# Kernel optimization log

Hardware: AMD Instinct MI355X
Metric: run time of the kernel (lower is better)

The kernel has to match this reference:

```python
import jax, jax.numpy as jnp
import numpy as np

BS, T, X_DIM = 16, 4096, 256


def setup_inputs() -> dict:
    key = jax.random.key(0)
    kx, kb, kl = jax.random.split(key, 3)
    x_set = jax.random.normal(kx, (BS, T, X_DIM), dtype=jnp.float32)
    # Match torch.nn.init.orthogonal_ via QR of a Gaussian matrix
    B, _ = jnp.linalg.qr(jax.random.normal(kb, (X_DIM, X_DIM), dtype=jnp.float32))
    Lam, _ = jnp.linalg.qr(jax.random.normal(kl, (X_DIM, X_DIM), dtype=jnp.float32))
    return {"x_set": x_set, "B": B.astype(jnp.float32), "Lam": Lam.astype(jnp.float32)}


def reference(x_set, B, Lam):
    # Original computes h_T = sum_{j=0}^{T} Lambda^j @ B @ x_{T-j} (O(T^2)).
    # Equivalent linear recurrence: h_t = Lambda @ h_{t-1} + B @ x_t, h_{-1} = 0.
    Bx = jnp.einsum('de,bte->btd', B, x_set)          # [bs, T, d]

    def step(h, bx_t):
        h = jnp.einsum('de,be->bd', Lam, h) + bx_t    # [bs, d]
        return h, h

    h0 = jnp.zeros((x_set.shape[0], x_set.shape[2]), dtype=x_set.dtype)
    _, hs = jax.lax.scan(step, h0, jnp.swapaxes(Bx, 0, 1))  # [T, bs, d]
    return jnp.swapaxes(hs, 0, 1)                            # [bs, T, d]
```

## Files before the change

### kernel.cpp

```cpp
#include <hip/hip_runtime.h>
#include <hip/hip_bf16.h>
#include <stdint.h>


#define CHUNK  64
#define NCHUNK 64

typedef short v8s __attribute__((ext_vector_type(8)));
typedef float v4f __attribute__((ext_vector_type(4)));

static __device__ __forceinline__ unsigned short f2u(float f) {
  union { float f; unsigned int u; } x; x.f = f;
  unsigned int u = x.u + 0x7FFFu + ((x.u >> 16) & 1u);
  return (unsigned short)(u >> 16);
}
static __device__ __forceinline__ float u2f(unsigned short h) {
  union { unsigned int u; float f; } x; x.u = ((unsigned int)h) << 16;
  return x.f;
}
static __device__ __forceinline__ void lds_barrier() {
  asm volatile("s_waitcnt lgkmcnt(0)\n\ts_barrier" ::: "memory");
}

template<bool A_F32, bool C_BF16, bool ADD_C>
__global__ __launch_bounds__(256) void gemm_tile(
    const void* __restrict__ Ap, const unsigned short* __restrict__ Bp,
    void* __restrict__ Cp, int lda, int ldb, int ldc, int Kper, long csplit)
{
  __shared__ unsigned short As[64][72];
  __shared__ unsigned short Bst[64][72];
  const int tid = threadIdx.x;
  const int lane = tid & 63, w = tid >> 6;
  const int q = lane >> 4, ln = lane & 15;
  const long n0 = (long)blockIdx.x * 64;
  const long m0 = (long)blockIdx.y * 64;
  const int  kz = blockIdx.z;
  const long kbase = (long)kz * Kper;
  const int sm = tid >> 2;
  const int sk = (tid & 3) << 4;

  v4f acc[4];
#pragma unroll
  for (int i = 0; i < 4; ++i) acc[i] = 0;

  float4 fA[4];
  v8s aR0, aR1, bR0, bR1;

  auto load_tile = [&](long kg) {
    if (A_F32) {
      const float* A = (const float*)Ap + (m0 + sm) * (long)lda + kg + sk;
#pragma unroll
      for (int t = 0; t < 4; ++t) fA[t] = ((const float4*)A)[t];
    } else {
      const unsigned short* A = (const unsigned short*)Ap + (m0 + sm) * (long)lda + kg + sk;
      aR0 = ((const v8s*)A)[0]; aR1 = ((const v8s*)A)[1];
    }
    const unsigned short* Bg = Bp + (kg + sm) * (long)ldb + n0 + sk;
    bR0 = ((const v8s*)Bg)[0]; bR1 = ((const v8s*)Bg)[1];
  };

  load_tile(kbase);

  for (int ks = 0; ks < Kper; ks += 64) {
    __syncthreads();
    if (A_F32) {
      unsigned short* d = &As[sm][sk];
#pragma unroll
      for (int t = 0; t < 4; ++t) {
        d[4*t+0] = f2u(fA[t].x); d[4*t+1] = f2u(fA[t].y);
        d[4*t+2] = f2u(fA[t].z); d[4*t+3] = f2u(fA[t].w);
      }
    } else {
      *(v8s*)&As[sm][sk] = aR0; *(v8s*)&As[sm][sk + 8] = aR1;
    }
#pragma unroll
    for (int r = 0; r < 8; ++r) Bst[sk + r][sm] = (unsigned short)bR0[r];
#pragma unroll
    for (int r = 0; r < 8; ++r) Bst[sk + 8 + r][sm] = (unsigned short)bR1[r];
    __syncthreads();
    if (ks + 64 < Kper) load_tile(kbase + ks + 64);
#pragma unroll
    for (int kb = 0; kb < 64; kb += 32) {
      v8s a = *(const v8s*)&As[w*16 + ln][kb + q*8];
#pragma unroll
      for (int nb = 0; nb < 4; ++nb) {
        v8s b = *(const v8s*)&Bst[nb*16 + ln][kb + q*8];
        acc[nb] = __builtin_amdgcn_mfma_f32_16x16x32_bf16(a, b, acc[nb], 0, 0, 0);
      }
    }
  }
#pragma unroll
  for (int nb = 0; nb < 4; ++nb)
#pragma unroll
    for (int r = 0; r < 4; ++r) {
      const long row = m0 + w*16 + q*4 + r;
      const long col = n0 + nb*16 + ln;
      float v = acc[nb][r];
      if (C_BF16) ((unsigned short*)Cp)[row * (long)ldc + col] = f2u(v);
      else {
        float* Cf = (float*)Cp + (long)kz * csplit;
        if (ADD_C) v += Cf[row * (long)ldc + col];
        Cf[row * (long)ldc + col] = v;
      }
    }
}

__global__ __launch_bounds__(256) void pow_round(
    unsigned short* __restrict__ Phi, unsigned short* __restrict__ Plo, int mpow)
{
  __shared__ unsigned short As[64][72];
  __shared__ unsigned short Bst[64][72];
  const int tid = threadIdx.x, lane = tid & 63, w = tid >> 6;
  const int q = lane >> 4, ln = lane & 15;
  const int jj = (blockIdx.x >> 2) + 1;
  const int n0 = (blockIdx.x & 3) * 64;
  const int m0 = blockIdx.y * 64;
  const unsigned short* Ah = Phi + (size_t)mpow * 65536;
  const unsigned short* Al = Plo + (size_t)mpow * 65536;
  const unsigned short* Bh = Phi + (size_t)jj * 65536;
  const unsigned short* Bl = Plo + (size_t)jj * 65536;
  const int sm = tid >> 2, sk = (tid & 3) << 4;
  v4f acc[4];
#pragma unroll
  for (int i = 0; i < 4; ++i) acc[i] = 0;

  v8s aR0, aR1, bR0, bR1;
  auto load_tile = [&](int it) {
    const int seg = it >> 2, ks = (it & 3) << 6;
    const unsigned short* Asrc = (seg == 1) ? Al : Ah;
    const unsigned short* Bsrc = (seg == 2) ? Bl : Bh;
    const unsigned short* Ag = Asrc + (size_t)(m0 + sm) * 256 + ks + sk;
    aR0 = ((const v8s*)Ag)[0]; aR1 = ((const v8s*)Ag)[1];
    const unsigned short* Bg = Bsrc + (size_t)(ks + sm) * 256 + n0 + sk;
    bR0 = ((const v8s*)Bg)[0]; bR1 = ((const v8s*)Bg)[1];
  };

  load_tile(0);
  for (int it = 0; it < 12; ++it) {
    __syncthreads();
    *(v8s*)&As[sm][sk] = aR0; *(v8s*)&As[sm][sk + 8] = aR1;
#pragma unroll
    for (int r = 0; r < 8; ++r) Bst[sk + r][sm] = (unsigned short)bR0[r];
#pragma unroll
    for (int r = 0; r < 8; ++r) Bst[sk + 8 + r][sm] = (unsigned short)bR1[r];
    __syncthreads();
    if (it + 1 < 12) load_tile(it + 1);
#pragma unroll
    for (int kb = 0; kb < 64; kb += 32) {
      v8s a = *(const v8s*)&As[w*16 + ln][kb + q*8];
#pragma unroll
      for (int nb = 0; nb < 4; ++nb) {
        v8s bb = *(const v8s*)&Bst[nb*16 + ln][kb + q*8];
        acc[nb] = __builtin_amdgcn_mfma_f32_16x16x32_bf16(a, bb, acc[nb], 0, 0, 0);
      }
    }
  }
  const size_t ob = (size_t)(mpow + jj) * 65536;
#pragma unroll
  for (int nb = 0; nb < 4; ++nb)
#pragma unroll
    for (int r = 0; r < 4; ++r) {
      const int row = m0 + w*16 + q*4 + r;
      const int col = n0 + nb*16 + ln;
      float v = acc[nb][r];
      unsigned short hi = f2u(v);
      Phi[ob + (size_t)row*256 + col] = hi;
      Plo[ob + (size_t)row*256 + col] = f2u(v - u2f(hi));
    }
}

__global__ __launch_bounds__(256) void pack_init(
    const float* __restrict__ Bm, const float* __restrict__ Lam,
    unsigned short* __restrict__ Bt, unsigned short* __restrict__ LamT,
    unsigned short* __restrict__ Phi, unsigned short* __restrict__ Plo)
{
  const int idx = blockIdx.x * 256 + threadIdx.x;
  const int e = idx >> 8, d = idx & 255;
  Bt[idx]   = f2u(Bm[d * 256 + e]);
  LamT[idx] = f2u(Lam[d * 256 + e]);
  float v = Lam[idx];
  unsigned short hi = f2u(v);
  Phi[65536 + idx] = hi;
  Plo[65536 + idx] = f2u(v - u2f(hi));
  const int dd = idx >> 8, ee = idx & 255;
  Phi[idx] = (dd == ee) ? (unsigned short)0x3F80 : (unsigned short)0;
  Plo[idx] = 0;
}

__global__ __launch_bounds__(256) void pack2_init(
    const unsigned short* __restrict__ Phi, const unsigned short* __restrict__ Plo,
    unsigned short* __restrict__ Phi2, unsigned short* __restrict__ Plo2)
{
  const int idx = blockIdx.x * 256 + threadIdx.x;
  const int dd = idx >> 8, ee = idx & 255;
  Phi2[idx] = (dd == ee) ? (unsigned short)0x3F80 : (unsigned short)0;
  Plo2[idx] = 0;
  Phi2[65536 + idx] = Phi[(size_t)64 * 65536 + idx];
  Plo2[65536 + idx] = Plo[(size_t)64 * 65536 + idx];
}

__global__ __launch_bounds__(256) void pack_all(
    const unsigned short* __restrict__ Phi,
    const unsigned short* __restrict__ Phi2, const unsigned short* __restrict__ Plo2,
    unsigned short* __restrict__ Ghat, unsigned short* __restrict__ Q,
    unsigned short* __restrict__ Qcat, unsigned short* __restrict__ G2,
    unsigned short* __restrict__ LcT2hi, unsigned short* __restrict__ LcT2lo)
{
  __shared__ unsigned short tile[64][65];
  const int tx = threadIdx.x & 63, ty = threadIdx.x >> 6;
  const int blk0 = blockIdx.x;
  if (blk0 < 2048) {
    const int blk = blk0;
    int t16, jpar;
    const unsigned short* src;
    if (blk < 1024) { jpar = blk >> 4;            t16 = blk & 15;  src = Phi + (size_t)(63 - jpar) * 65536; }
    else            { int v = blk - 1024; jpar = v >> 4; t16 = v & 15; src = Phi + (size_t)(jpar + 1) * 65536; }
    const int d0 = (t16 & 3) * 64, e0 = (t16 >> 2) * 64;
#pragma unroll
    for (int s = 0; s < 16; ++s)
      tile[ty*16 + s][tx] = src[(size_t)(d0 + ty*16 + s) * 256 + e0 + tx];
    __syncthreads();
    if (blk < 1024) {
#pragma unroll
      for (int s = 0; s < 16; ++s) {
        const int e = e0 + ty*16 + s, d = d0 + tx;
        Ghat[((size_t)(jpar*256 + e)) * 256 + d] = tile[tx][ty*16 + s];
      }
    } else {
#pragma unroll
      for (int s = 0; s < 16; ++s) {
        const int e = e0 + ty*16 + s, d = d0 + tx;
        Q[(size_t)e * 16384 + jpar*256 + d] = tile[tx][ty*16 + s];
      }
    }
    return;
  }
  const int blk = blk0 - 2048;
  if (blk < 1152) {
    const int rt = blk >> 5, ct = blk & 31;
    const int k0 = rt * 64, c0 = ct * 64;
    const int r = c0 >> 8, d0 = c0 & 255;
    int p = 0, e0 = 0;
    bool zero = false;
    if (k0 < 256) { p = r; e0 = k0; }
    else {
      const int u = (k0 - 256) >> 8; e0 = (k0 - 256) & 255;
      if (u >= r) zero = true; else p = r - 1 - u;
    }
    if (zero) {
#pragma unroll
      for (int s = 0; s < 16; ++s)
        Qcat[(size_t)(k0 + ty*16 + s) * 2048 + c0 + tx] = 0;
      return;
    }
    const unsigned short* src = Phi2 + (size_t)p * 65536;
#pragma unroll
    for (int s = 0; s < 16; ++s)
      tile[ty*16 + s][tx] = src[(size_t)(d0 + ty*16 + s) * 256 + e0 + tx];
    __syncthreads();
#pragma unroll
    for (int s = 0; s < 16; ++s)
      Qcat[(size_t)(k0 + ty*16 + s) * 2048 + c0 + tx] = tile[tx][ty*16 + s];
  } else if (blk < 1280) {
    const int t = blk - 1152;
    const int rt = t >> 2, ct = t & 3;
    const int k0 = rt * 64, d0 = ct * 64;
    const int r = k0 >> 8, e0 = k0 & 255;
    const unsigned short* src = Phi2 + (size_t)(7 - r) * 65536;
#pragma unroll
    for (int s = 0; s < 16; ++s)
      tile[ty*16 + s][tx] = src[(size_t)(d0 + ty*16 + s) * 256 + e0 + tx];
    __syncthreads();
#pragma unroll
    for (int s = 0; s < 16; ++s)
      G2[(size_t)(k0 + ty*16 + s) * 256 + d0 + tx] = tile[tx][ty*16 + s];
  } else {
    const int t = blk - 1280;
    const int half = t >> 4, t16 = t & 15;
    const int d0 = (t16 & 3) * 64, e0 = (t16 >> 2) * 64;
    const unsigned short* src = (half ? Plo2 : Phi2) + (size_t)8 * 65536;
    unsigned short* dst = half ? LcT2lo : LcT2hi;
#pragma unroll
    for (int s = 0; s < 16; ++s)
      tile[ty*16 + s][tx] = src[(size_t)(d0 + ty*16 + s) * 256 + e0 + tx];
    __syncthreads();
#pragma unroll
    for (int s = 0; s < 16; ++s)
      dst[(size_t)(e0 + ty*16 + s) * 256 + d0 + tx] = tile[tx][ty*16 + s];
  }
}

__global__ __launch_bounds__(256) void reduce_s2(
    const float* __restrict__ Sp, unsigned short* __restrict__ Acat)
{
  const int f = blockIdx.x * 256 + threadIdx.x;
  float v = 0;
#pragma unroll
  for (int z = 0; z < 8; ++z) v += Sp[(size_t)z * 262144 + f];
  const int e = f & 255, i = (f >> 8) & 63, b = f >> 14;
  const int u = i & 7, m = i >> 3;
  Acat[(size_t)(b*8 + m) * 2304 + 256 + u*256 + e] = f2u(v);
}

__global__ __launch_bounds__(512, 2) void k4b_combine(
    const unsigned short* __restrict__ LcT2hi, const unsigned short* __restrict__ LcT2lo,
    const float* __restrict__ S2, unsigned short* __restrict__ Acat)
{
  __shared__ unsigned short Hhi[16][264];
  __shared__ unsigned short Hlo[16][264];
  const int tid = threadIdx.x, lane = tid & 63, w = tid >> 6;
  const int q = lane >> 4, ln = lane & 15;

  v8s bhi[8][2], blo[8][2];
#pragma unroll
  for (int kk = 0; kk < 8; ++kk)
#pragma unroll
    for (int nb = 0; nb < 2; ++nb) {
      const int n = 32*w + nb*16 + ln;
#pragma unroll
      for (int r = 0; r < 8; ++r) {
        const int k = kk*32 + q*8 + r;
        bhi[kk][nb][r] = (short)LcT2hi[k*256 + n];
        blo[kk][nb][r] = (short)LcT2lo[k*256 + n];
      }
    }
  for (int e = tid; e < 16*264; e += 512) { (&Hhi[0][0])[e] = 0; (&Hlo[0][0])[e] = 0; }
  lds_barrier();

  for (int m = 0; m < 8; ++m) {
    for (int e = tid; e < 4096; e += 512) {
      const int b = e >> 8, d = e & 255;
      Acat[(size_t)(b*8 + m) * 2304 + d] = Hhi[b][d];
    }
    v8s ahi[8], alo[8];
#pragma unroll
    for (int kk = 0; kk < 8; ++kk) {
      ahi[kk] = *(const v8s*)&Hhi[ln][kk*32 + q*8];
      alo[kk] = *(const v8s*)&Hlo[ln][kk*32 + q*8];
    }
    lds_barrier();
    v4f acc[2];
#pragma unroll
    for (int nb = 0; nb < 2; ++nb)
#pragma unroll
      for (int r = 0; r < 4; ++r) {
        const int bb = 4*q + r, col = 32*w + nb*16 + ln;
        acc[nb][r] = S2[(size_t)(bb*8 + m) * 256 + col];
      }
#pragma unroll
    for (int kk = 0; kk < 8; ++kk)
#pragma unroll
      for (int nb = 0; nb < 2; ++nb) {
        acc[nb] = __builtin_amdgcn_mfma_f32_16x16x32_bf16(ahi[kk], bhi[kk][nb], acc[nb], 0, 0, 0);
        acc[nb] = __builtin_amdgcn_mfma_f32_16x16x32_bf16(alo[kk], bhi[kk][nb], acc[nb], 0, 0, 0);
        acc[nb] = __builtin_amdgcn_mfma_f32_16x16x32_bf16(ahi[kk], blo[kk][nb], acc[nb], 0, 0, 0);
      }
#pragma unroll
    for (int nb = 0; nb < 2; ++nb)
#pragma unroll
      for (int r = 0; r < 4; ++r) {
        const int bb = 4*q + r, col = 32*w + nb*16 + ln;
        float v = acc[nb][r];
        unsigned short hi = f2u(v);
        Hhi[bb][col] = hi;
        Hlo[bb][col] = f2u(v - u2f(hi));
      }
    lds_barrier();
  }
}

__global__ __launch_bounds__(256, 1) void k5_scan(
    const unsigned short* __restrict__ LamT,
    const unsigned short* __restrict__ Bx, float* __restrict__ Out)
{
  __shared__ unsigned short gs[2][16][264];
  const int tid = threadIdx.x, lane = tid & 63, w = tid >> 6;
  const int q = lane >> 4, ln = lane & 15;
  const int blk = blockIdx.x;
  const int b  = blk >> 4;
  const int i0 = (blk * 4) & 63;

  v8s bf[8][4];
#pragma unroll
  for (int kk = 0; kk < 8; ++kk)
#pragma unroll
    for (int nb = 0; nb < 4; ++nb) {
      const int n = 64*w + nb*16 + ln;
#pragma unroll
      for (int r = 0; r < 8; ++r)
        bf[kk][nb][r] = (short)LamT[(kk*32 + q*8 + r) * 256 + n];
    }
  for (int e = tid; e < 16*264; e += 256) (&gs[0][0][0])[e] = 0;

  size_t base[4];
#pragma unroll
  for (int r = 0; r < 4; ++r)
    base[r] = ((size_t)b*4096 + (size_t)(i0 + r)*64) * 256;
  const int colw = 64*w;

  unsigned short bxr[2][4][4];
  if (q == 0) {
#pragma unroll
    for (int s = 0; s < 2; ++s)
#pragma unroll
      for (int r = 0; r < 4; ++r)
#pragma unroll
        for (int nb = 0; nb < 4; ++nb)
          bxr[s][r][nb] = Bx[base[r] + (size_t)s*256 + colw + nb*16 + ln];
  }
  lds_barrier();

#pragma unroll 2
  for (int j = 0; j < CHUNK; ++j) {
    v8s a[8];
#pragma unroll
    for (int kk = 0; kk < 8; ++kk) a[kk] = *(const v8s*)&gs[j & 1][ln][kk*32 + q*8];
    v4f acc[4];
#pragma unroll
    for (int nb = 0; nb < 4; ++nb) acc[nb] = 0;
#pragma unroll
    for (int kk = 0; kk < 8; ++kk)
#pragma unroll
      for (int nb = 0; nb < 4; ++nb)
        acc[nb] = __builtin_amdgcn_mfma_f32_16x16x32_bf16(a[kk], bf[kk][nb], acc[nb], 0, 0, 0);
    if (q == 0) {
#pragma unroll
      for (int r = 0; r < 4; ++r) {
        const size_t rb = base[r] + (size_t)j*256 + colw;
#pragma unroll
        for (int nb = 0; nb < 4; ++nb) {
          const float g = acc[nb][r] + u2f(bxr[j & 1][r][nb]);
          Out[rb + nb*16 + ln] = g;
          gs[(j + 1) & 1][r][colw + nb*16 + ln] = f2u(g);
        }
      }
      if (j < CHUNK - 2) {
#pragma unroll
        for (int r = 0; r < 4; ++r) {
          const size_t rb = base[r] + (size_t)(j + 2)*256 + colw;
#pragma unroll
          for (int nb = 0; nb < 4; ++nb)
            bxr[j & 1][r][nb] = Bx[rb + nb*16 + ln];
        }
      }
    }
    lds_barrier();
  }
}

extern "C" void kernel_launch(void* const* d_in, const int* in_sizes, int n_in,
                              void* d_out, int out_size, void* d_ws, size_t ws_size,
                              hipStream_t stream)
{
  const float* x   = (const float*)d_in[0];
  const float* Bm  = (const float*)d_in[1];
  const float* Lam = (const float*)d_in[2];
  float* Out = (float*)d_out;
  (void)in_sizes; (void)n_in; (void)out_size; (void)ws_size;

  char* ws = (char*)d_ws;
  size_t off = 0;
  auto alloc = [&](size_t bytes) { void* p = ws + off; off += (bytes + 255) & ~(size_t)255; return p; };
  unsigned short* Bx    = (unsigned short*)alloc((size_t)16777216 * 2);
  unsigned short* Phi   = (unsigned short*)alloc((size_t)65 * 65536 * 2);
  unsigned short* Plo   = (unsigned short*)alloc((size_t)65 * 65536 * 2);
  unsigned short* Ghat  = (unsigned short*)alloc((size_t)16384 * 256 * 2);
  unsigned short* Q     = (unsigned short*)alloc((size_t)256 * 16384 * 2);
  unsigned short* Qcat  = (unsigned short*)alloc((size_t)2304 * 2048 * 2);
  unsigned short* G2    = (unsigned short*)alloc((size_t)2048 * 256 * 2);
  unsigned short* Phi2  = (unsigned short*)alloc((size_t)9 * 65536 * 2);
  unsigned short* Plo2  = (unsigned short*)alloc((size_t)9 * 65536 * 2);
  unsigned short* Bt    = (unsigned short*)alloc(131072);
  unsigned short* LamT  = (unsigned short*)alloc(131072);
  unsigned short* LcT2hi= (unsigned short*)alloc(131072);
  unsigned short* LcT2lo= (unsigned short*)alloc(131072);
  unsigned short* Acat  = (unsigned short*)alloc((size_t)128 * 2304 * 2);
  float*          S2    = (float*)alloc(131072);
  unsigned short* Abf   = (unsigned short*)alloc(524288);
  float*          Spart = (float*)Plo;

  pack_init<<<dim3(256), dim3(256), 0, stream>>>(Bm, Lam, Bt, LamT, Phi, Plo);
  gemm_tile<true, true, false><<<dim3(4, 1024, 1), dim3(256), 0, stream>>>(
      (const void*)x, Bt, (void*)Bx, 256, 256, 256, 256, 0);
  k5_scan<<<dim3(256), dim3(256), 0, stream>>>(LamT, Bx, Out);
  for (int mp = 1; mp <= 32; mp <<= 1)
    pow_round<<<dim3(mp * 4, 4, 1), dim3(256), 0, stream>>>(Phi, Plo, mp);
  pack2_init<<<dim3(256), dim3(256), 0, stream>>>(Phi, Plo, Phi2, Plo2);
  for (int mp = 1; mp <= 4; mp <<= 1)
    pow_round<<<dim3(mp * 4, 4, 1), dim3(256), 0, stream>>>(Phi2, Plo2, mp);
  pack_all<<<dim3(3360), dim3(256), 0, stream>>>(Phi, Phi2, Plo2,
      Ghat, Q, Qcat, G2, LcT2hi, LcT2lo);
  gemm_tile<false, false, false><<<dim3(4, 16, 8), dim3(256), 0, stream>>>(
      (const void*)Bx, Ghat, (void*)Spart, 16384, 256, 256, 2048, 262144);
  reduce_s2<<<dim3(1024), dim3(256), 0, stream>>>(Spart, Acat);
  gemm_tile<false, false, false><<<dim3(4, 2, 1), dim3(256), 0, stream>>>(
      (const void*)(Acat + 256), G2, (void*)S2, 2304, 256, 256, 2048, 0);
  k4b_combine<<<dim3(1), dim3(512), 0, stream>>>(LcT2hi, LcT2lo, S2, Acat);
  gemm_tile<false, true, false><<<dim3(32, 2, 1), dim3(256), 0, stream>>>(
      (const void*)Acat, Qcat, (void*)Abf, 2304, 2048, 2048, 2304, 0);
  gemm_tile<false, false, true><<<dim3(256, 16, 1), dim3(256), 0, stream>>>(
      (const void*)Abf, Q, (void*)Out, 256, 16384, 16384, 256, 0);
}
```

Baseline: 433.4 us.

## Merge power-doubling launches into persistent kernel and fuse split-K reduction

Replaces the nine separate pow_round launches and the pack2_init launch with one persistent kernel of 128 blocks. The blocks step through the doubling rounds using atomic-counter grid barriers. The split-K GEMM now does its own reduction: the last block to finish each output tile, found with an atomic ticket, sums the 8 partials and writes bf16 into Acat, so the reduce_s2 launch goes away. This removes launch overhead and idle gaps between small dependent kernels. The cost is spin-wait barriers, which assume all 128 blocks are co-resident, plus extra atomics and counter setup.

```diff
diff --git a/kernel.cpp b/kernel.cpp
--- a/kernel.cpp
+++ b/kernel.cpp
@@ -4,7 +4,7 @@
 
 
 #define CHUNK  64
-#define NCHUNK 64
+#define NPB    128
 
 typedef short v8s __attribute__((ext_vector_type(8)));
 typedef float v4f __attribute__((ext_vector_type(4)));
@@ -20,6 +20,17 @@
 }
 static __device__ __forceinline__ void lds_barrier() {
   asm volatile("s_waitcnt lgkmcnt(0)\n\ts_barrier" ::: "memory");
+}
+static __device__ __forceinline__ void gbar(unsigned* c) {
+  __threadfence();
+  __syncthreads();
+  if (threadIdx.x == 0) {
+    atomicAdd(c, 1u);
+    while (__hip_atomic_load(c, __ATOMIC_RELAXED, __HIP_MEMORY_SCOPE_AGENT) < NPB)
+      __builtin_amdgcn_s_sleep(2);
+    __threadfence();
+  }
+  __syncthreads();
 }
 
 template<bool A_F32, bool C_BF16, bool ADD_C>
@@ -105,38 +116,35 @@
     }
 }
 
-__global__ __launch_bounds__(256) void pow_round(
-    unsigned short* __restrict__ Phi, unsigned short* __restrict__ Plo, int mpow)
+__global__ __launch_bounds__(256) void gemm_sum(
+    const unsigned short* __restrict__ Bx, const unsigned short* __restrict__ Ghat,
+    float* __restrict__ Spart, unsigned short* __restrict__ Acat,
+    unsigned int* __restrict__ tilecnt)
 {
   __shared__ unsigned short As[64][72];
   __shared__ unsigned short Bst[64][72];
+  __shared__ unsigned int oldsh;
   const int tid = threadIdx.x, lane = tid & 63, w = tid >> 6;
   const int q = lane >> 4, ln = lane & 15;
-  const int jj = (blockIdx.x >> 2) + 1;
-  const int n0 = (blockIdx.x & 3) * 64;
-  const int m0 = blockIdx.y * 64;
-  const unsigned short* Ah = Phi + (size_t)mpow * 65536;
-  const unsigned short* Al = Plo + (size_t)mpow * 65536;
-  const unsigned short* Bh = Phi + (size_t)jj * 65536;
-  const unsigned short* Bl = Plo + (size_t)jj * 65536;
+  const long n0 = (long)blockIdx.x * 64;
+  const long m0 = (long)blockIdx.y * 64;
+  const int  kz = blockIdx.z;
+  const long kbase = (long)kz * 2048;
   const int sm = tid >> 2, sk = (tid & 3) << 4;
   v4f acc[4];
 #pragma unroll
   for (int i = 0; i < 4; ++i) acc[i] = 0;
 
   v8s aR0, aR1, bR0, bR1;
-  auto load_tile = [&](int it) {
-    const int seg = it >> 2, ks = (it & 3) << 6;
-    const unsigned short* Asrc = (seg == 1) ? Al : Ah;
-    const unsigned short* Bsrc = (seg == 2) ? Bl : Bh;
-    const unsigned short* Ag = Asrc + (size_t)(m0 + sm) * 256 + ks + sk;
-    aR0 = ((const v8s*)Ag)[0]; aR1 = ((const v8s*)Ag)[1];
-    const unsigned short* Bg = Bsrc + (size_t)(ks + sm) * 256 + n0 + sk;
+  auto load_tile = [&](long kg) {
+    const unsigned short* A = Bx + (m0 + sm) * 16384L + kg + sk;
+    aR0 = ((const v8s*)A)[0]; aR1 = ((const v8s*)A)[1];
+    const unsigned short* Bg = Ghat + (kg + sm) * 256L + n0 + sk;
     bR0 = ((const v8s*)Bg)[0]; bR1 = ((const v8s*)Bg)[1];
   };
 
-  load_tile(0);
-  for (int it = 0; it < 12; ++it) {
+  load_tile(kbase);
+  for (int ks = 0; ks < 2048; ks += 64) {
     __syncthreads();
     *(v8s*)&As[sm][sk] = aR0; *(v8s*)&As[sm][sk + 8] = aR1;
 #pragma unroll
@@ -144,36 +152,56 @@
 #pragma unroll
     for (int r = 0; r < 8; ++r) Bst[sk + 8 + r][sm] = (unsigned short)bR1[r];
     __syncthreads();
-    if (it + 1 < 12) load_tile(it + 1);
+    if (ks + 64 < 2048) load_tile(kbase + ks + 64);
 #pragma unroll
     for (int kb = 0; kb < 64; kb += 32) {
       v8s a = *(const v8s*)&As[w*16 + ln][kb + q*8];
 #pragma unroll
       for (int nb = 0; nb < 4; ++nb) {
-        v8s bb = *(const v8s*)&Bst[nb*16 + ln][kb + q*8];
-        acc[nb] = __builtin_amdgcn_mfma_f32_16x16x32_bf16(a, bb, acc[nb], 0, 0, 0);
-      }
-    }
-  }
-  const size_t ob = (size_t)(mpow + jj) * 65536;
+        v8s b = *(const v8s*)&Bst[nb*16 + ln][kb + q*8];
+        acc[nb] = __builtin_amdgcn_mfma_f32_16x16x32_bf16(a, b, acc[nb], 0, 0, 0);
+      }
+    }
+  }
 #pragma unroll
   for (int nb = 0; nb < 4; ++nb)
 #pragma unroll
     for (int r = 0; r < 4; ++r) {
-      const int row = m0 + w*16 + q*4 + r;
-      const int col = n0 + nb*16 + ln;
-      float v = acc[nb][r];
-      unsigned short hi = f2u(v);
-      Phi[ob + (size_t)row*256 + col] = hi;
-      Plo[ob + (size_t)row*256 + col] = f2u(v - u2f(hi));
-    }
+      const long row = m0 + w*16 + q*4 + r;
+      const long col = n0 + nb*16 + ln;
+      Spart[(long)kz * 262144 + row * 256 + col] = acc[nb][r];
+    }
+  __threadfence();
+  __syncthreads();
+  if (tid == 0)
+    oldsh = __hip_atomic_fetch_add(&tilecnt[blockIdx.y * 4 + blockIdx.x], 1u,
+                                   __ATOMIC_ACQ_REL, __HIP_MEMORY_SCOPE_AGENT);
+  __syncthreads();
+  if (oldsh == 7) {
+    __threadfence();
+#pragma unroll
+    for (int nb = 0; nb < 4; ++nb)
+#pragma unroll
+      for (int r = 0; r < 4; ++r) {
+        const long row = m0 + w*16 + q*4 + r;
+        const long col = n0 + nb*16 + ln;
+        float v = 0;
+#pragma unroll
+        for (int z = 0; z < 8; ++z) v += Spart[(long)z * 262144 + row * 256 + col];
+        const int b = (int)(row >> 6), i = (int)(row & 63);
+        const int u = i & 7, m = i >> 3;
+        Acat[(size_t)(b*8 + m) * 2304 + 256 + u*256 + (int)col] = f2u(v);
+      }
+  }
 }
 
 __global__ __launch_bounds__(256) void pack_init(
     const float* __restrict__ Bm, const float* __restrict__ Lam,
     unsigned short* __restrict__ Bt, unsigned short* __restrict__ LamT,
-    unsigned short* __restrict__ Phi, unsigned short* __restrict__ Plo)
-{
+    unsigned short* __restrict__ Phi, unsigned short* __restrict__ Plo,
+    unsigned int* __restrict__ cnt)
+{
+  if (blockIdx.x == 0 && threadIdx.x < 128) cnt[threadIdx.x] = 0;
   const int idx = blockIdx.x * 256 + threadIdx.x;
   const int e = idx >> 8, d = idx & 255;
   Bt[idx]   = f2u(Bm[d * 256 + e]);
@@ -187,16 +215,99 @@
   Plo[idx] = 0;
 }
 
-__global__ __launch_bounds__(256) void pack2_init(
-    const unsigned short* __restrict__ Phi, const unsigned short* __restrict__ Plo,
-    unsigned short* __restrict__ Phi2, unsigned short* __restrict__ Plo2)
-{
-  const int idx = blockIdx.x * 256 + threadIdx.x;
-  const int dd = idx >> 8, ee = idx & 255;
-  Phi2[idx] = (dd == ee) ? (unsigned short)0x3F80 : (unsigned short)0;
-  Plo2[idx] = 0;
-  Phi2[65536 + idx] = Phi[(size_t)64 * 65536 + idx];
-  Plo2[65536 + idx] = Plo[(size_t)64 * 65536 + idx];
+static __device__ __forceinline__ void pow_job(
+    unsigned short* __restrict__ Phi, unsigned short* __restrict__ Plo,
+    int mpow, int job,
+    unsigned short (*As)[72], unsigned short (*Bst)[72])
+{
+  const int tid = threadIdx.x, lane = tid & 63, w = tid >> 6;
+  const int q = lane >> 4, ln = lane & 15;
+  const int jj = (job >> 4) + 1;
+  const int n0 = (job & 3) * 64;
+  const int m0 = ((job >> 2) & 3) * 64;
+  const unsigned short* Ah = Phi + (size_t)mpow * 65536;
+  const unsigned short* Al = Plo + (size_t)mpow * 65536;
+  const unsigned short* Bh = Phi + (size_t)jj * 65536;
+  const unsigned short* Bl = Plo + (size_t)jj * 65536;
+  const int sm = tid >> 2, sk = (tid & 3) << 4;
+  v4f acc[4];
+#pragma unroll
+  for (int i = 0; i < 4; ++i) acc[i] = 0;
+
+  v8s aR0, aR1, bR0, bR1;
+  auto load_tile = [&](int it) {
+    const int seg = it >> 2, ks = (it & 3) << 6;
+    const unsigned short* Asrc = (seg == 1) ? Al : Ah;
+    const unsigned short* Bsrc = (seg == 2) ? Bl : Bh;
+    const unsigned short* Ag = Asrc + (size_t)(m0 + sm) * 256 + ks + sk;
+    aR0 = ((const v8s*)Ag)[0]; aR1 = ((const v8s*)Ag)[1];
+    const unsigned short* Bg = Bsrc + (size_t)(ks + sm) * 256 + n0 + sk;
+    bR0 = ((const v8s*)Bg)[0]; bR1 = ((const v8s*)Bg)[1];
+  };
+
+  load_tile(0);
+  for (int it = 0; it < 12; ++it) {
+    __syncthreads();
+    *(v8s*)&As[sm][sk] = aR0; *(v8s*)&As[sm][sk + 8] = aR1;
+#pragma unroll
+    for (int r = 0; r < 8; ++r) Bst[sk + r][sm] = (unsigned short)bR0[r];
+#pragma unroll
+    for (int r = 0; r < 8; ++r) Bst[sk + 8 + r][sm] = (unsigned short)bR1[r];
+    __syncthreads();
+    if (it + 1 < 12) load_tile(it + 1);
+#pragma unroll
+    for (int kb = 0; kb < 64; kb += 32) {
+      v8s a = *(const v8s*)&As[w*16 + ln][kb + q*8];
+#pragma unroll
+      for (int nb = 0; nb < 4; ++nb) {
+        v8s bb = *(const v8s*)&Bst[nb*16 + ln][kb + q*8];
+        acc[nb] = __builtin_amdgcn_mfma_f32_16x16x32_bf16(a, bb, acc[nb], 0, 0, 0);
+      }
+    }
+  }
+  const size_t ob = (size_t)(mpow + jj) * 65536;
+#pragma unroll
+  for (int nb = 0; nb < 4; ++nb)
+#pragma unroll
+    for (int r = 0; r < 4; ++r) {
+      const int row = m0 + w*16 + q*4 + r;
+      const int col = n0 + nb*16 + ln;
+      float v = acc[nb][r];
+      unsigned short hi = f2u(v);
+      Phi[ob + (size_t)row*256 + col] = hi;
+      Plo[ob + (size_t)row*256 + col] = f2u(v - u2f(hi));
+    }
+}
+
+__global__ __launch_bounds__(256) void pow_chain(
+    unsigned short* __restrict__ Phi,  unsigned short* __restrict__ Plo,
+    unsigned short* __restrict__ Phi2, unsigned short* __restrict__ Plo2,
+    unsigned int* __restrict__ cnt)
+{
+  __shared__ unsigned short As[64][72];
+  __shared__ unsigned short Bst[64][72];
+  const int pid = blockIdx.x, tid = threadIdx.x;
+  int bar = 0;
+#pragma unroll 1
+  for (int mp = 1; mp <= 32; mp <<= 1) {
+    for (int job = pid; job < 16 * mp; job += NPB)
+      pow_job(Phi, Plo, mp, job, As, Bst);
+    gbar(&cnt[bar++]);
+  }
+  for (int idx = pid * 256 + tid; idx < 65536; idx += NPB * 256) {
+    const int dd = idx >> 8, ee = idx & 255;
+    Phi2[idx] = (dd == ee) ? (unsigned short)0x3F80 : (unsigned short)0;
+    Plo2[idx] = 0;
+    Phi2[65536 + idx] = Phi[(size_t)64 * 65536 + idx];
+    Plo2[65536 + idx] = Plo[(size_t)64 * 65536 + idx];
+  }
+  gbar(&cnt[bar++]);
+#pragma unroll 1
+  for (int mp = 1; mp <= 4; mp <<= 1) {
+    for (int job = pid; job < 16 * mp; job += NPB)
+      pow_job(Phi2, Plo2, mp, job, As, Bst);
+    gbar(&cnt[bar++]);
+  }
 }
 
 __global__ __launch_bounds__(256) void pack_all(
@@ -288,18 +399,6 @@
     for (int s = 0; s < 16; ++s)
       dst[(size_t)(e0 + ty*16 + s) * 256 + d0 + tx] = tile[tx][ty*16 + s];
   }
-}
-
-__global__ __launch_bounds__(256) void reduce_s2(
-    const float* __restrict__ Sp, unsigned short* __restrict__ Acat)
-{
-  const int f = blockIdx.x * 256 + threadIdx.x;
-  float v = 0;
-#pragma unroll
-  for (int z = 0; z < 8; ++z) v += Sp[(size_t)z * 262144 + f];
-  const int e = f & 255, i = (f >> 8) & 63, b = f >> 14;
-  const int u = i & 7, m = i >> 3;
-  Acat[(size_t)(b*8 + m) * 2304 + 256 + u*256 + e] = f2u(v);
 }
 
 __global__ __launch_bounds__(512, 2) void k4b_combine(
@@ -477,22 +576,17 @@
   unsigned short* Acat  = (unsigned short*)alloc((size_t)128 * 2304 * 2);
   float*          S2    = (float*)alloc(131072);
   unsigned short* Abf   = (unsigned short*)alloc(524288);
+  unsigned int*   cnt   = (unsigned int*)alloc(512);
   float*          Spart = (float*)Plo;
 
-  pack_init<<<dim3(256), dim3(256), 0, stream>>>(Bm, Lam, Bt, LamT, Phi, Plo);
+  pack_init<<<dim3(256), dim3(256), 0, stream>>>(Bm, Lam, Bt, LamT, Phi, Plo, cnt);
   gemm_tile<true, true, false><<<dim3(4, 1024, 1), dim3(256), 0, stream>>>(
       (const void*)x, Bt, (void*)Bx, 256, 256, 256, 256, 0);
   k5_scan<<<dim3(256), dim3(256), 0, stream>>>(LamT, Bx, Out);
-  for (int mp = 1; mp <= 32; mp <<= 1)
-    pow_round<<<dim3(mp * 4, 4, 1), dim3(256), 0, stream>>>(Phi, Plo, mp);
-  pack2_init<<<dim3(256), dim3(256), 0, stream>>>(Phi, Plo, Phi2, Plo2);
-  for (int mp = 1; mp <= 4; mp <<= 1)
-    pow_round<<<dim3(mp * 4, 4, 1), dim3(256), 0, stream>>>(Phi2, Plo2, mp);
+  pow_chain<<<dim3(NPB), dim3(256), 0, stream>>>(Phi, Plo, Phi2, Plo2, cnt);
   pack_all<<<dim3(3360), dim3(256), 0, stream>>>(Phi, Phi2, Plo2,
       Ghat, Q, Qcat, G2, LcT2hi, LcT2lo);
-  gemm_tile<false, false, false><<<dim3(4, 16, 8), dim3(256), 0, stream>>>(
-      (const void*)Bx, Ghat, (void*)Spart, 16384, 256, 256, 2048, 262144);
-  reduce_s2<<<dim3(1024), dim3(256), 0, stream>>>(Spart, Acat);
+  gemm_sum<<<dim3(4, 16, 8), dim3(256), 0, stream>>>(Bx, Ghat, Spart, Acat, cnt + 32);
   gemm_tile<false, false, false><<<dim3(4, 2, 1), dim3(256), 0, stream>>>(
       (const void*)(Acat + 256), G2, (void*)S2, 2304, 256, 256, 2048, 0);
   k4b_combine<<<dim3(1), dim3(512), 0, stream>>>(LcT2hi, LcT2lo, S2, Acat);
```

Measured after the change: 677.0 us. 56.2% more time.
